# Performance work log

Measured on AMD Instinct MI355X. Metric: run time of the kernel, lower is better.

Reference implementation:

```python
import jax, jax.numpy as jnp
import numpy as np

DECAY = 0.99
EPSILON = 1e-05
CODEBOOK_SIZE = 1024
DIM = 128


def setup_inputs() -> dict:
    key = jax.random.key(0)
    k1, k2, k3, k4 = jax.random.split(key, 4)
    x = jax.random.normal(k1, (8, 8192, DIM), dtype=jnp.float32)
    embed = jax.random.normal(k2, (CODEBOOK_SIZE, DIM), dtype=jnp.float32)
    cluster_size = jax.random.uniform(k3, (CODEBOOK_SIZE,), dtype=jnp.float32)
    embed_avg = jax.random.normal(k4, (CODEBOOK_SIZE, DIM), dtype=jnp.float32)
    return {"x": x, "embed": embed, "cluster_size": cluster_size, "embed_avg": embed_avg}


def reference(x, embed, cluster_size, embed_avg):
    shape = x.shape
    flat = x.reshape(-1, shape[-1])  # [N, dim]

    # quantize: negative squared euclidean distance, argmax == nearest code
    dist = -(jnp.sum(flat * flat, axis=1, keepdims=True)
             - 2.0 * flat @ embed.T
             + jnp.sum(embed * embed, axis=1)[None, :])  # [N, K]
    embed_ind = jnp.argmax(dist, axis=-1)  # [N]

    quantize = embed[embed_ind].reshape(shape)            # dequantize
    embed_ind_out = embed_ind.reshape(shape[:-1])

    # training-time EMA updates (one-hot expressed as segment_sum)
    batch_cluster_size = jax.ops.segment_sum(
        jnp.ones_like(embed_ind, dtype=flat.dtype), embed_ind,
        num_segments=CODEBOOK_SIZE)                       # == one_hot.sum(0)
    new_cluster_size = cluster_size * DECAY + (1.0 - DECAY) * batch_cluster_size

    embed_sum = jax.ops.segment_sum(flat, embed_ind,
                                    num_segments=CODEBOOK_SIZE)  # == (x.T @ one_hot).T
    new_embed_avg = embed_avg * DECAY + (1.0 - DECAY) * embed_sum

    total = new_cluster_size.sum()
    smoothed = (new_cluster_size + EPSILON) / (total + CODEBOOK_SIZE * EPSILON)
    smoothed_counts = smoothed * total
    new_embed = new_embed_avg / smoothed_counts[:, None]

    return quantize, embed_ind_out, new_cluster_size, new_embed_avg, new_embed
```

## Files before the change

### kernel.cpp

```cpp
#include <hip/hip_runtime.h>
#include <math.h>

#define DIM 128
#define KCODES 1024
#define NROWS 65536

typedef short bf16x8 __attribute__((ext_vector_type(8)));
typedef float f32x4 __attribute__((ext_vector_type(4)));

#define WS_COUNTS 0
#define WS_ESUM   1024
#define WS_IOFF   132096
#define WS_TOTAL  133120
#define WS_ENORM2 133124
#define WS_EBF    134148
#define WS_WIN    461828
#define WS_SORTED 527364
#define WS_SCODE  592900

#define OFF_Q   0
#define OFF_IND 8388608
#define OFF_NCS 8454144
#define OFF_NEA 8455168
#define OFF_NE  8586240

static __device__ __forceinline__ unsigned short f2bf(float f) {
    unsigned u = __float_as_uint(f);
    unsigned r = (u + 0x7FFFu + ((u >> 16) & 1u)) >> 16;
    return (unsigned short)r;
}

__global__ __launch_bounds__(64) void k_prep(const float* __restrict__ embed,
                                             unsigned short* __restrict__ ebf,
                                             float* __restrict__ en2,
                                             float* __restrict__ counts,
                                             float* __restrict__ esum,
                                             int* __restrict__ cursor) {
    int k = blockIdx.x;
    int l = threadIdx.x;
    if (l == 0) { counts[k] = 0.0f; cursor[k] = 0; }
    *(float2*)&esum[(size_t)k * DIM + l * 2] = (float2){0.0f, 0.0f};
    float2 v = *(const float2*)&embed[(size_t)k * DIM + l * 2];
    ushort2 b;
    b.x = f2bf(v.x);
    b.y = f2bf(v.y);
    *(ushort2*)&ebf[k * DIM + l * 2] = b;
    float s = v.x * v.x + v.y * v.y;
    #pragma unroll
    for (int off = 32; off; off >>= 1) s += __shfl_xor(s, off);
    if (l == 0) en2[k] = 512.0f - 0.5f * s;
}

__global__ __launch_bounds__(512, 4) void k_fused(const float* __restrict__ x,
                                                  const float* __restrict__ embed,
                                                  const unsigned short* __restrict__ ebf,
                                                  const float* __restrict__ en2g,
                                                  int* __restrict__ win_g,
                                                  float* __restrict__ counts,
                                                  float* __restrict__ out) {
    __shared__ unsigned short buf[2][128 * 128];
    __shared__ float en2s[KCODES];
    __shared__ int winS[128];

    const int tid = threadIdx.x;
    const int row0 = blockIdx.x * 128;

    #pragma unroll
    for (int i = 0; i < 2; ++i) en2s[i * 512 + tid] = en2g[i * 512 + tid];

    #pragma unroll
    for (int i = 0; i < 8; ++i) {
        int idx4 = i * 512 + tid;
        int lin = idx4 * 4;
        int r = lin >> 7, d = lin & 127;
        float4 v = *(const float4*)&x[(size_t)(row0 + r) * DIM + d];
        ushort4 b;
        b.x = f2bf(v.x); b.y = f2bf(v.y); b.z = f2bf(v.z); b.w = f2bf(v.w);
        *(ushort4*)&buf[0][(r * 128 + d) ^ ((r & 7) << 3)] = b;
    }
    __syncthreads();

    const int lane = tid & 63;
    const int wv = tid >> 6;
    const int ch = wv & 1;
    const int rh = (wv >> 1) * 32;
    const int l15 = lane & 15;
    const int q = lane >> 4;
    const int swz = (l15 & 7) << 3;

    bf16x8 af[4][2];
    #pragma unroll
    for (int ks = 0; ks < 4; ++ks)
        #pragma unroll
        for (int t = 0; t < 2; ++t)
            af[ks][t] = *(const bf16x8*)&buf[0][((rh + t * 16 + l15) * 128 + ks * 32 + q * 8) ^ swz];

    uint4 er[4];
    #pragma unroll
    for (int i = 0; i < 4; ++i) {
        int idx8 = i * 512 + tid;
        int r = idx8 >> 4;
        int d = (idx8 & 15) * 8;
        er[i] = *(const uint4*)&ebf[(size_t)r * DIM + d];
    }
    #pragma unroll
    for (int i = 0; i < 4; ++i) {
        int idx8 = i * 512 + tid;
        int r = idx8 >> 4;
        int d = (idx8 & 15) * 8;
        *(uint4*)&buf[1][(r * 128 + d) ^ ((r & 7) << 3)] = er[i];
    }
    __syncthreads();

    float m1[2][4], m2[2][4];
    #pragma unroll
    for (int a = 0; a < 2; ++a)
        #pragma unroll
        for (int b = 0; b < 4; ++b) { m1[a][b] = 0.0f; m2[a][b] = 0.0f; }

    for (int ct = 0; ct < 8; ++ct) {
        const int c0 = ct * 128;
        const unsigned short* cbuf = buf[1 ^ (ct & 1)];

        if (ct < 7) {
            #pragma unroll
            for (int i = 0; i < 4; ++i) {
                int idx8 = i * 512 + tid;
                int r = idx8 >> 4;
                int d = (idx8 & 15) * 8;
                er[i] = *(const uint4*)&ebf[(size_t)(c0 + 128 + r) * DIM + d];
            }
        }

        f32x4 acc[2][4];
        #pragma unroll
        for (int cl = 0; cl < 4; ++cl) {
            float en = en2s[c0 + ch * 64 + cl * 16 + l15];
            #pragma unroll
            for (int rt = 0; rt < 2; ++rt) acc[rt][cl] = (f32x4){en, en, en, en};
        }

        __builtin_amdgcn_s_setprio(1);
        #pragma unroll
        for (int ks = 0; ks < 4; ++ks) {
            bf16x8 bfr[4];
            #pragma unroll
            for (int cl = 0; cl < 4; ++cl)
                bfr[cl] = *(const bf16x8*)&cbuf[((ch * 64 + cl * 16 + l15) * 128 + ks * 32 + q * 8) ^ swz];
            #pragma unroll
            for (int rt = 0; rt < 2; ++rt)
                #pragma unroll
                for (int cl = 0; cl < 4; ++cl)
                    acc[rt][cl] = __builtin_amdgcn_mfma_f32_16x16x32_bf16(af[ks][rt], bfr[cl],
                                                                          acc[rt][cl], 0, 0, 0);
        }

        #pragma unroll
        for (int cp = 0; cp < 2; ++cp) {
            unsigned cu0 = (unsigned)(c0 + ch * 64 + cp * 32 + l15);
            unsigned cu1 = cu0 + 16u;
            #pragma unroll
            for (int rt = 0; rt < 2; ++rt)
                #pragma unroll
                for (int rg = 0; rg < 4; ++rg) {
                    float sa = acc[rt][cp * 2][rg];
                    float sb = acc[rt][cp * 2 + 1][rg];
                    float a = __uint_as_float((__float_as_uint(sa) & ~1023u) | cu0);
                    float b = __uint_as_float((__float_as_uint(sb) & ~1023u) | cu1);
                    m2[rt][rg] = fmaxf(m2[rt][rg],
                                       __builtin_amdgcn_fmed3f(a, b, m1[rt][rg]));
                    m1[rt][rg] = fmaxf(fmaxf(a, b), m1[rt][rg]);
                }
        }
        __builtin_amdgcn_s_setprio(0);

        if (ct < 7) {
            unsigned short* nbuf = buf[ct & 1];
            #pragma unroll
            for (int i = 0; i < 4; ++i) {
                int idx8 = i * 512 + tid;
                int r = idx8 >> 4;
                int d = (idx8 & 15) * 8;
                *(uint4*)&nbuf[(r * 128 + d) ^ ((r & 7) << 3)] = er[i];
            }
        }
        __syncthreads();
    }

    float* scratch = (float*)buf[0];
    unsigned* hist = (unsigned*)buf[0] + 512;

    #pragma unroll
    for (int rt = 0; rt < 2; ++rt)
        #pragma unroll
        for (int rg = 0; rg < 4; ++rg) {
            float a1 = m1[rt][rg], a2 = m2[rt][rg];
            #pragma unroll
            for (int off = 1; off <= 8; off <<= 1) {
                float o1 = __shfl_xor(a1, off);
                float o2 = __shfl_xor(a2, off);
                float t = fmaxf(a2, o2);
                a2 = __builtin_amdgcn_fmed3f(a1, o1, t);
                a1 = fmaxf(a1, o1);
            }
            if (l15 == 0) {
                int row = rh + rt * 16 + q * 4 + rg;
                scratch[row * 4 + ch * 2 + 0] = a1;
                scratch[row * 4 + ch * 2 + 1] = a2;
            }
        }

    #pragma unroll
    for (int i = 0; i < 2; ++i) hist[i * 512 + tid] = 0u;
    __syncthreads();

    {
        const int sub = tid & 15;
        const int g = tid >> 4;
        #pragma unroll 2
        for (int rr = 0; rr < 4; ++rr) {
            const int lrow = g * 4 + rr;
            const float* sp = &scratch[lrow * 4];
            int ci[4];
            ci[0] = (int)(__float_as_uint(sp[0]) & 1023u);
            ci[1] = (int)(__float_as_uint(sp[1]) & 1023u);
            ci[2] = (int)(__float_as_uint(sp[2]) & 1023u);
            ci[3] = (int)(__float_as_uint(sp[3]) & 1023u);

            const float* xr = &x[(size_t)(row0 + lrow) * DIM + sub * 4];
            float4 xa = *(const float4*)xr;
            float4 xb = *(const float4*)(xr + 64);

            double d[4];
            #pragma unroll
            for (int j = 0; j < 4; ++j) {
                const float* er2 = &embed[(size_t)ci[j] * DIM + sub * 4];
                float4 ea4 = *(const float4*)er2;
                float4 eb4 = *(const float4*)(er2 + 64);
                double t0 = (double)xa.x - (double)ea4.x;
                double t1 = (double)xa.y - (double)ea4.y;
                double t2 = (double)xa.z - (double)ea4.z;
                double t3 = (double)xa.w - (double)ea4.w;
                double t4 = (double)xb.x - (double)eb4.x;
                double t5 = (double)xb.y - (double)eb4.y;
                double t6 = (double)xb.z - (double)eb4.z;
                double t7 = (double)xb.w - (double)eb4.w;
                d[j] = ((t0 * t0 + t1 * t1) + (t2 * t2 + t3 * t3)) +
                       ((t4 * t4 + t5 * t5) + (t6 * t6 + t7 * t7));
            }
            #pragma unroll
            for (int off = 1; off <= 8; off <<= 1) {
                #pragma unroll
                for (int j = 0; j < 4; ++j) d[j] += __shfl_xor(d[j], off);
            }

            int win = ci[0];
            double dw = d[0];
            #pragma unroll
            for (int j = 1; j < 4; ++j) {
                bool b = (d[j] < dw) || (d[j] == dw && ci[j] < win);
                dw = b ? d[j] : dw;
                win = b ? ci[j] : win;
            }
            if (sub == 0) winS[lrow] = win;
        }
    }
    __syncthreads();

    if (tid < 128) {
        int w = winS[tid];
        atomicAdd(&hist[w], 1u);
        win_g[row0 + tid] = w;
        out[OFF_IND + row0 + tid] = (float)w;
    }

    #pragma unroll 4
    for (int i = 0; i < 16; ++i) {
        int lrow = wv * 16 + i;
        int w = winS[lrow];
        float2 v = *(const float2*)&embed[(size_t)w * DIM + lane * 2];
        *(float2*)&out[OFF_Q + (size_t)(row0 + lrow) * DIM + lane * 2] = v;
    }

    __syncthreads();
    #pragma unroll
    for (int i = 0; i < 2; ++i) {
        unsigned c = hist[i * 512 + tid];
        if (c) atomicAdd(&counts[i * 512 + tid], (float)c);
    }
}

__global__ __launch_bounds__(1024) void k_scansort(const float* __restrict__ cs,
                                                   const int* __restrict__ win_arr,
                                                   float* __restrict__ ws,
                                                   int* __restrict__ sorted,
                                                   int* __restrict__ scode,
                                                   float* __restrict__ out) {
    __shared__ int h[KCODES];
    __shared__ int bs[KCODES];
    __shared__ int wsum[16];
    __shared__ float wtot[16];
    const float* counts = ws + WS_COUNTS;
    int* cursor = (int*)(ws + WS_IOFF);

    const int t = threadIdx.x;
    h[t] = 0;
    __syncthreads();
    const int row = blockIdx.x * 1024 + t;
    const int w = win_arr[row];
    const int r = atomicAdd(&h[w], 1);

    const int lane = t & 63, wvi = t >> 6;
    const float cf = counts[t];
    const int c = (int)cf;
    int v = c;
    #pragma unroll
    for (int off = 1; off < 64; off <<= 1) {
        int o = __shfl_up(v, off);
        if (lane >= off) v += o;
    }
    if (lane == 63) wsum[wvi] = v;
    if (blockIdx.x == 0) {
        float ncs = cs[t] * 0.99f + 0.01f * cf;
        out[OFF_NCS + t] = ncs;
        float nf = ncs;
        #pragma unroll
        for (int off = 32; off; off >>= 1) nf += __shfl_xor(nf, off);
        if (lane == 0) wtot[wvi] = nf;
    }
    __syncthreads();

    int base = 0;
    for (int i = 0; i < wvi; ++i) base += wsum[i];
    const int gbase = base + v - c;

    if (blockIdx.x == 0 && t == 0) {
        float tt = 0.f;
        for (int i = 0; i < 16; ++i) tt += wtot[i];
        ws[WS_TOTAL] = tt;
    }

    const int cnt = h[t];
    if (cnt) bs[t] = gbase + atomicAdd(&cursor[t], cnt);
    __syncthreads();
    const int pos = bs[w] + r;
    sorted[pos] = row;
    scode[pos] = w;
}

__global__ __launch_bounds__(256) void k_segsum(const float* __restrict__ x,
                                                const int* __restrict__ sorted,
                                                const int* __restrict__ scode,
                                                float* __restrict__ esum) {
    const int lane = threadIdx.x & 63;
    const int wv = threadIdx.x >> 6;
    const int base = blockIdx.x * 256 + wv * 64;
    const int l15 = lane & 15;

    float ax = 0.f, ay = 0.f;
    int cur = -1;

    #pragma unroll
    for (int cc = 0; cc < 4; ++cc) {
        const int p = base + cc * 16 + l15;
        const int srow = sorted[p];
        const int sc = scode[p];
        if (cc == 0) cur = __shfl(sc, 0);
        #pragma unroll
        for (int j = 0; j < 16; ++j) {
            int row = __shfl(srow, j);
            int c = __shfl(sc, j);
            if (c != cur) {
                atomicAdd(&esum[cur * DIM + lane * 2], ax);
                atomicAdd(&esum[cur * DIM + lane * 2 + 1], ay);
                ax = 0.f; ay = 0.f;
                cur = c;
            }
            float2 v = *(const float2*)&x[(size_t)row * DIM + lane * 2];
            ax += v.x;
            ay += v.y;
        }
    }
    atomicAdd(&esum[cur * DIM + lane * 2], ax);
    atomicAdd(&esum[cur * DIM + lane * 2 + 1], ay);
}

__global__ __launch_bounds__(256) void k_embed(const float* __restrict__ ea,
                                               const float* __restrict__ ws,
                                               float* __restrict__ out) {
    int i = blockIdx.x * 256 + threadIdx.x;
    int k = i >> 7;
    float nea = ea[i] * 0.99f + 0.01f * ws[WS_ESUM + i];
    out[OFF_NEA + i] = nea;
    float total = ws[WS_TOTAL];
    float ncs = out[OFF_NCS + k];
    float sm = (ncs + 1e-5f) / (total + 1024.0f * 1e-5f);
    out[OFF_NE + i] = nea / (sm * total);
}

extern "C" void kernel_launch(void* const* d_in, const int* in_sizes, int n_in,
                              void* d_out, int out_size, void* d_ws, size_t ws_size,
                              hipStream_t stream) {
    const float* x     = (const float*)d_in[0];
    const float* embed = (const float*)d_in[1];
    const float* cs    = (const float*)d_in[2];
    const float* ea    = (const float*)d_in[3];
    float* out = (float*)d_out;
    float* ws  = (float*)d_ws;

    k_prep<<<KCODES, 64, 0, stream>>>(embed, (unsigned short*)(ws + WS_EBF),
                                      ws + WS_ENORM2, ws + WS_COUNTS, ws + WS_ESUM,
                                      (int*)(ws + WS_IOFF));
    k_fused<<<NROWS / 128, 512, 0, stream>>>(x, embed,
                                             (const unsigned short*)(ws + WS_EBF),
                                             ws + WS_ENORM2, (int*)(ws + WS_WIN),
                                             ws + WS_COUNTS, out);
    k_scansort<<<NROWS / 1024, 1024, 0, stream>>>(cs, (const int*)(ws + WS_WIN), ws,
                                                  (int*)(ws + WS_SORTED),
                                                  (int*)(ws + WS_SCODE), out);
    k_segsum<<<NROWS / 256, 256, 0, stream>>>(x, (const int*)(ws + WS_SORTED),
                                              (const int*)(ws + WS_SCODE), ws + WS_ESUM);
    k_embed<<<131072 / 256, 256, 0, stream>>>(ea, ws, out);
}
```

Before: 152.7 us.

## Load codebook tiles directly into LDS via global_load_lds with pre-swizzled layout

The bf16 codebook is now stored pre-swizzled in global memory by the prep kernel, so each 128-code tile can be copied straight into shared memory with 16-byte global_load_lds instructions. This replaces the path through registers (global load into VGPRs, then LDS store after the MFMA loop). It aims to cut VGPR pressure and instruction count and to overlap the next tile's fetch with compute. It depends on the direct-to-LDS writes being complete by the existing __syncthreads and on the ebf layout change matching every other reader of ebf.

```diff
diff --git a/kernel.cpp b/kernel.cpp
--- a/kernel.cpp
+++ b/kernel.cpp
@@ -28,6 +28,13 @@
     unsigned u = __float_as_uint(f);
     unsigned r = (u + 0x7FFFu + ((u >> 16) & 1u)) >> 16;
     return (unsigned short)r;
+}
+
+static __device__ __forceinline__ void gload_lds16(const unsigned short* g,
+                                                   unsigned short* l) {
+    __builtin_amdgcn_global_load_lds(
+        (const __attribute__((address_space(1))) void*)g,
+        (__attribute__((address_space(3))) void*)l, 16, 0, 0);
 }
 
 __global__ __launch_bounds__(64) void k_prep(const float* __restrict__ embed,
@@ -44,7 +51,7 @@
     ushort2 b;
     b.x = f2bf(v.x);
     b.y = f2bf(v.y);
-    *(ushort2*)&ebf[k * DIM + l * 2] = b;
+    *(ushort2*)&ebf[(k * DIM + l * 2) ^ ((k & 7) << 3)] = b;
     float s = v.x * v.x + v.y * v.y;
     #pragma unroll
     for (int off = 32; off; off >>= 1) s += __shfl_xor(s, off);
@@ -88,28 +95,18 @@
     const int q = lane >> 4;
     const int swz = (l15 & 7) << 3;
 
+    #pragma unroll
+    for (int i = 0; i < 4; ++i) {
+        int idx8 = i * 512 + tid;
+        gload_lds16(&ebf[idx8 * 8], &buf[1][idx8 * 8]);
+    }
+
     bf16x8 af[4][2];
     #pragma unroll
     for (int ks = 0; ks < 4; ++ks)
         #pragma unroll
         for (int t = 0; t < 2; ++t)
             af[ks][t] = *(const bf16x8*)&buf[0][((rh + t * 16 + l15) * 128 + ks * 32 + q * 8) ^ swz];
-
-    uint4 er[4];
-    #pragma unroll
-    for (int i = 0; i < 4; ++i) {
-        int idx8 = i * 512 + tid;
-        int r = idx8 >> 4;
-        int d = (idx8 & 15) * 8;
-        er[i] = *(const uint4*)&ebf[(size_t)r * DIM + d];
-    }
-    #pragma unroll
-    for (int i = 0; i < 4; ++i) {
-        int idx8 = i * 512 + tid;
-        int r = idx8 >> 4;
-        int d = (idx8 & 15) * 8;
-        *(uint4*)&buf[1][(r * 128 + d) ^ ((r & 7) << 3)] = er[i];
-    }
     __syncthreads();
 
     float m1[2][4], m2[2][4];
@@ -123,12 +120,12 @@
         const unsigned short* cbuf = buf[1 ^ (ct & 1)];
 
         if (ct < 7) {
+            unsigned short* nbuf = buf[ct & 1];
+            const unsigned short* gsrc = ebf + (size_t)(c0 + 128) * DIM;
             #pragma unroll
             for (int i = 0; i < 4; ++i) {
                 int idx8 = i * 512 + tid;
-                int r = idx8 >> 4;
-                int d = (idx8 & 15) * 8;
-                er[i] = *(const uint4*)&ebf[(size_t)(c0 + 128 + r) * DIM + d];
+                gload_lds16(&gsrc[idx8 * 8], &nbuf[idx8 * 8]);
             }
         }
 
@@ -174,16 +171,6 @@
         }
         __builtin_amdgcn_s_setprio(0);
 
-        if (ct < 7) {
-            unsigned short* nbuf = buf[ct & 1];
-            #pragma unroll
-            for (int i = 0; i < 4; ++i) {
-                int idx8 = i * 512 + tid;
-                int r = idx8 >> 4;
-                int d = (idx8 & 15) * 8;
-                *(uint4*)&nbuf[(r * 128 + d) ^ ((r & 7) << 3)] = er[i];
-            }
-        }
         __syncthreads();
     }
 
```

Measured after the change: 152.8 us. Within noise of the previous version (+0.0%).
